# Performance work log

Hardware: AMD Instinct MI355X
Metric: run time of the kernel (lower is better)

## Reference

```python
import jax, jax.numpy as jnp
import numpy as np

# Model dims
B, T, E, H = 2, 2048, 512, 8
HEAD_DIM = E // H            # 64
NUM_SCALES = 4               # Gauss-Laguerre quadrature nodes
NUM_PRF = 16                 # positive random features per scale
POLY_DIM = 16                # degree-2 TensorSketch dim
EPS = 1e-5
CHUNK = 128                  # chunk size for exact chunked causal linear attention


def setup_inputs() -> dict:
    key = jax.random.key(0)
    ks = jax.random.split(key, 10)
    x = jax.random.normal(ks[0], (B, T, E), jnp.float32)
    sc = 1.0 / np.sqrt(E)  # xavier-ish scale for square projections
    Wq = jax.random.normal(ks[1], (E, E), jnp.float32) * sc
    Wk = jax.random.normal(ks[2], (E, E), jnp.float32) * sc
    Wv = jax.random.normal(ks[3], (E, E), jnp.float32) * sc
    Wo = jax.random.normal(ks[4], (E, E), jnp.float32) * sc
    # FAVOR+ gaussian projections, one block per quadrature scale
    projections = jax.random.normal(ks[5], (NUM_SCALES, NUM_PRF, HEAD_DIM), jnp.float32)
    # Gauss-Laguerre nodes/weights for 1/(C - 2 q.k) = int_0^inf exp(-t(C - 2 q.k)) dt
    nodes, weights = np.polynomial.laguerre.laggauss(NUM_SCALES)
    coef = weights * np.exp(nodes) * np.exp(-nodes * EPS)
    scales = jnp.asarray(np.stack([nodes, coef], axis=1), jnp.float32)  # [S, 2] = (t_s, c_s)
    # degree-2 TensorSketch (count-sketch hashes + rademacher signs)
    sketch_h = jax.random.randint(ks[6], (2, HEAD_DIM), 0, POLY_DIM)
    sketch_s = (jax.random.randint(ks[7], (2, HEAD_DIM), 0, 2) * 2 - 1).astype(jnp.float32)
    return dict(x=x, Wq=Wq, Wk=Wk, Wv=Wv, Wo=Wo, projections=projections,
                scales=scales, sketch_h=sketch_h, sketch_s=sketch_s)


def _features(u, projections, scales, sketch_h, sketch_s):
    """Multi-scale FAVOR+ x TensorSketch feature map for the spherical YAT kernel.

    u: [B,T,H,d], unit-normalized along d. Returns [B,T,H, P*S*m].
    Phi(q).Phi(k) ~= (q.k)^2 / (||q-k||^2 + eps).
    """
    t = scales[:, 0]  # quadrature nodes t_s
    c = scales[:, 1]  # quadrature coeffs w_s e^{t_s} e^{-t_s eps}
    S, m, d = projections.shape
    z = jnp.einsum('smd,bthd->bthsm', projections, u)
    # exp(2 t q.k) via positive RFs; extra e^{-t||u||^2}=e^{-t} (unit sphere) folded in -> -2t
    ef = jnp.exp(jnp.sqrt(2.0 * t)[:, None] * z - 2.0 * t[:, None]) * jnp.sqrt(c / m)[:, None]  # [B,T,H,S,m]
    # degree-2 TensorSketch: countsketch via one-hot matmul, combine with FFT conv
    M1 = sketch_s[0][:, None] * jax.nn.one_hot(sketch_h[0], POLY_DIM, dtype=u.dtype)  # [d,P]
    M2 = sketch_s[1][:, None] * jax.nn.one_hot(sketch_h[1], POLY_DIM, dtype=u.dtype)
    ts = jnp.fft.irfft(jnp.fft.rfft(u @ M1) * jnp.fft.rfft(u @ M2), n=POLY_DIM)  # [B,T,H,P]
    Bs, Ts, Hs = u.shape[:3]
    ef = ef.reshape(Bs, Ts, Hs, S * m)
    return (ts[..., :, None] * ef[..., None, :]).reshape(Bs, Ts, Hs, POLY_DIM * S * m)


def reference(x, Wq, Wk, Wv, Wo, projections, scales, sketch_h, sketch_s):
    Bx, Tx, Ex = x.shape
    d = HEAD_DIM
    q = (x @ Wq).reshape(Bx, Tx, H, d)
    k = (x @ Wk).reshape(Bx, Tx, H, d)
    v = (x @ Wv).reshape(Bx, Tx, H, d)
    # spherical: project q,k to unit sphere
    qn = q / (jnp.linalg.norm(q, axis=-1, keepdims=True) + 1e-6)
    kn = k / (jnp.linalg.norm(k, axis=-1, keepdims=True) + 1e-6)
    fq = _features(qn, projections, scales, sketch_h, sketch_s)  # [B,T,H,F]
    fk = _features(kn, projections, scales, sketch_h, sketch_s)
    F = fq.shape[-1]
    # exact chunked causal linear attention: O(T) state, no [T,T] matrix
    N = Tx // CHUNK
    fq_ = fq.reshape(Bx, N, CHUNK, H, F)
    fk_ = fk.reshape(Bx, N, CHUNK, H, F)
    v_ = v.reshape(Bx, N, CHUNK, H, d)
    kv = jnp.einsum('bnchf,bnchd->bnhfd', fk_, v_)   # per-chunk sum of phi(k) v^T
    kz = fk_.sum(axis=2)                              # [B,N,H,F]
    kv_prev = jnp.concatenate([jnp.zeros_like(kv[:, :1]), jnp.cumsum(kv, axis=1)[:, :-1]], axis=1)
    kz_prev = jnp.concatenate([jnp.zeros_like(kz[:, :1]), jnp.cumsum(kz, axis=1)[:, :-1]], axis=1)
    num = jnp.einsum('bnchf,bnhfd->bnchd', fq_, kv_prev)
    den = jnp.einsum('bnchf,bnhf->bnch', fq_, kz_prev)
    # intra-chunk causal part
    sc = jnp.einsum('bnchf,bnkhf->bnhck', fq_, fk_)
    mask = jnp.tril(jnp.ones((CHUNK, CHUNK), bool))
    scm = jnp.where(mask, sc, 0.0)
    num = num + jnp.einsum('bnhck,bnkhd->bnchd', scm, v_)
    den = den + jnp.swapaxes(scm.sum(axis=-1), 2, 3)
    out = num / (den[..., None] + EPS)
    out = out.reshape(Bx, Tx, Ex) @ Wo
    return out
```

## Files before the change

### kernel.cpp

```cpp
#include <hip/hip_runtime.h>
#include <math.h>

#define B_ 2
#define T_ 2048
#define E_ 512
#define H_ 8
#define D_ 64
#define NCH 16
#define CH 128
#define EPS_ 1e-5f

__global__ __launch_bounds__(256) void gemm512(const float* __restrict__ A,
                                               const float* __restrict__ W,
                                               float* __restrict__ C) {
  __shared__ float As[16][68];
  __shared__ float Bs[16][68];
  const int tid = threadIdx.x;
  const int tx = tid & 15, ty = tid >> 4;
  const int row0 = blockIdx.x * 64, col0 = blockIdx.y * 64;
  const int lr = tid >> 2, lk = (tid & 3) * 4;
  const int bkr = tid >> 4, bcc = (tid & 15) * 4;
  float acc[4][4] = {};
  for (int k0 = 0; k0 < 512; k0 += 16) {
    float4 a4 = *(const float4*)(A + (size_t)(row0 + lr) * 512 + k0 + lk);
    As[lk + 0][lr] = a4.x; As[lk + 1][lr] = a4.y;
    As[lk + 2][lr] = a4.z; As[lk + 3][lr] = a4.w;
    *(float4*)&Bs[bkr][bcc] = *(const float4*)(W + (size_t)(k0 + bkr) * 512 + col0 + bcc);
    __syncthreads();
#pragma unroll
    for (int kk = 0; kk < 16; ++kk) {
      float4 av = *(const float4*)&As[kk][ty * 4];
      float4 bv = *(const float4*)&Bs[kk][tx * 4];
      float aa[4] = {av.x, av.y, av.z, av.w};
      float bb[4] = {bv.x, bv.y, bv.z, bv.w};
#pragma unroll
      for (int i = 0; i < 4; ++i)
#pragma unroll
        for (int j = 0; j < 4; ++j) acc[i][j] += aa[i] * bb[j];
    }
    __syncthreads();
  }
#pragma unroll
  for (int i = 0; i < 4; ++i) {
    float4 o = make_float4(acc[i][0], acc[i][1], acc[i][2], acc[i][3]);
    *(float4*)(C + (size_t)(row0 + ty * 4 + i) * 512 + col0 + tx * 4) = o;
  }
}

__global__ __launch_bounds__(256) void feat_kernel(
    const float* __restrict__ q, const float* __restrict__ k,
    const float* __restrict__ proj, const float* __restrict__ scales,
    const int* __restrict__ sh, const float* __restrict__ ss,
    float* __restrict__ Tq, float* __restrict__ Eq,
    float* __restrict__ Tk, float* __restrict__ Ek) {
  __shared__ float Us[128][68];
  __shared__ float PjT[64][68];
  __shared__ float MT[64][36];
  __shared__ float Ps[128][36];
  __shared__ float csq[64], cmb[64], ccf[64];
  const int tid = threadIdx.x;
  const int isK = blockIdx.y;
  const float* in = (isK ? k : q) + (size_t)blockIdx.x * 8192;
  float* To = isK ? Tk : Tq;
  float* Eo = isK ? Ek : Eq;

#pragma unroll
  for (int j = 0; j < 8; ++j) {
    const int f = tid + 256 * j;
    float4 a = *(const float4*)(in + 4 * f);
    *(float4*)&Us[f >> 4][(f & 15) * 4] = a;
  }
  for (int i = tid; i < 4096; i += 256) PjT[i & 63][i >> 6] = proj[i];
  for (int i = tid; i < 64 * 36; i += 256) (&MT[0][0])[i] = 0.f;
  __syncthreads();

  if (tid < 64) {
    MT[tid][sh[tid]] = ss[tid];
    MT[tid][16 + sh[64 + tid]] = ss[64 + tid];
  } else if (tid < 128) {
    const int c = tid - 64;
    const float t = scales[(c >> 4) * 2], cc = scales[(c >> 4) * 2 + 1];
    csq[c] = sqrtf(2.f * t); cmb[c] = -2.f * t; ccf[c] = sqrtf(cc / 16.f);
  }
  {
    const int r2 = tid >> 1, hf = tid & 1;
    float4 tv[8]; float s2 = 0.f;
#pragma unroll
    for (int j2 = 0; j2 < 8; ++j2) {
      tv[j2] = *(const float4*)&Us[r2][hf * 32 + 4 * j2];
      s2 += tv[j2].x * tv[j2].x + tv[j2].y * tv[j2].y + tv[j2].z * tv[j2].z + tv[j2].w * tv[j2].w;
    }
    s2 += __shfl_xor(s2, 1);
    const float inv = 1.f / (sqrtf(s2) + 1e-6f);
#pragma unroll
    for (int j2 = 0; j2 < 8; ++j2) {
      tv[j2].x *= inv; tv[j2].y *= inv; tv[j2].z *= inv; tv[j2].w *= inv;
      *(float4*)&Us[r2][hf * 32 + 4 * j2] = tv[j2];
    }
  }
  __syncthreads();

  const int tx = tid & 7, ty = tid >> 3;
  const int c0 = tx * 8, pc0 = tx * 4;
  float accz[4][8] = {};
  float accp[4][4] = {};
  for (int d0 = 0; d0 < 64; d0 += 4) {
    float Aar[4][4];
#pragma unroll
    for (int i = 0; i < 4; ++i) {
      float4 a4 = *(const float4*)&Us[ty + 32 * i][d0];
      Aar[i][0] = a4.x; Aar[i][1] = a4.y; Aar[i][2] = a4.z; Aar[i][3] = a4.w;
    }
#pragma unroll
    for (int dd = 0; dd < 4; ++dd) {
      float4 bl = *(const float4*)&PjT[d0 + dd][c0];
      float4 bh = *(const float4*)&PjT[d0 + dd][c0 + 4];
      float4 bm = *(const float4*)&MT[d0 + dd][pc0];
      float bb[8] = {bl.x, bl.y, bl.z, bl.w, bh.x, bh.y, bh.z, bh.w};
      float bp[4] = {bm.x, bm.y, bm.z, bm.w};
#pragma unroll
      for (int i = 0; i < 4; ++i) {
        const float a = Aar[i][dd];
#pragma unroll
        for (int j = 0; j < 8; ++j) accz[i][j] += a * bb[j];
#pragma unroll
        for (int j = 0; j < 4; ++j) accp[i][j] += a * bp[j];
      }
    }
  }

  float sq8[8], mb8[8], cf8[8];
#pragma unroll
  for (int j = 0; j < 8; ++j) { sq8[j] = csq[c0 + j]; mb8[j] = cmb[c0 + j]; cf8[j] = ccf[c0 + j]; }
  const int bx16 = blockIdx.x * 16;
#pragma unroll
  for (int i = 0; i < 4; ++i) {
    const int r = ty + 32 * i;
    const int bt = bx16 + (r >> 3);
    const size_t orow = (size_t)((bt >> 11) * 8 + (r & 7)) * 2048 + (bt & 2047);
    float e[8];
#pragma unroll
    for (int j = 0; j < 8; ++j) e[j] = expf(sq8[j] * accz[i][j] + mb8[j]) * cf8[j];
    *(float4*)(Eo + orow * 64 + c0) = make_float4(e[0], e[1], e[2], e[3]);
    *(float4*)(Eo + orow * 64 + c0 + 4) = make_float4(e[4], e[5], e[6], e[7]);
    *(float4*)&Ps[r][pc0] = make_float4(accp[i][0], accp[i][1], accp[i][2], accp[i][3]);
  }
  __syncthreads();

  const int rr = tid >> 1, hf2 = tid & 1;
  float p1v[16], p2v[16];
#pragma unroll
  for (int j4 = 0; j4 < 4; ++j4) {
    float4 a = *(const float4*)&Ps[rr][j4 * 4];
    p1v[j4 * 4 + 0] = a.x; p1v[j4 * 4 + 1] = a.y; p1v[j4 * 4 + 2] = a.z; p1v[j4 * 4 + 3] = a.w;
    float4 b2 = *(const float4*)&Ps[rr][16 + j4 * 4];
    p2v[j4 * 4 + 0] = b2.x; p2v[j4 * 4 + 1] = b2.y; p2v[j4 * 4 + 2] = b2.z; p2v[j4 * 4 + 3] = b2.w;
  }
  const int bt2 = bx16 + (rr >> 3);
  const size_t orow2 = (size_t)((bt2 >> 11) * 8 + (rr & 7)) * 2048 + (bt2 & 2047);
  float tout[8];
  if (hf2 == 0) {
#pragma unroll
    for (int r8 = 0; r8 < 8; ++r8) {
      float a = 0.f;
#pragma unroll
      for (int j = 0; j < 16; ++j) a += p1v[j] * p2v[(r8 - j) & 15];
      tout[r8] = a;
    }
  } else {
#pragma unroll
    for (int r8 = 0; r8 < 8; ++r8) {
      float a = 0.f;
#pragma unroll
      for (int j = 0; j < 16; ++j) a += p1v[j] * p2v[(8 + r8 - j) & 15];
      tout[r8] = a;
    }
  }
  *(float4*)(To + orow2 * 16 + hf2 * 8) = make_float4(tout[0], tout[1], tout[2], tout[3]);
  *(float4*)(To + orow2 * 16 + hf2 * 8 + 4) = make_float4(tout[4], tout[5], tout[6], tout[7]);
}

__global__ __launch_bounds__(256) void vrelayout(const float* __restrict__ v, float* __restrict__ vh) {
  const int f = blockIdx.x * 256 + threadIdx.x;
  float4 a = *(const float4*)(v + 4 * (size_t)f);
  const int d4 = f & 15, h = (f >> 4) & 7, bt = f >> 7;
  const size_t orow = (size_t)((bt >> 11) * 8 + h) * 2048 + (bt & 2047);
  *(float4*)(vh + orow * 64 + d4 * 4) = a;
}

__global__ __launch_bounds__(256) void kv_kernel(const float* __restrict__ Tk, const float* __restrict__ Ek,
                                                 const float* __restrict__ vh, float* __restrict__ KV) {
  const int bhn = blockIdx.x;
  const int slice = blockIdx.y;
  __shared__ float tks[128][20];
  __shared__ float eks[128][16];
  __shared__ float vs[128][64];
  const int tid = threadIdx.x;
  const size_t rowbase = (size_t)bhn * 128;
  for (int i = tid; i < 2048; i += 256) tks[i >> 4][i & 15] = Tk[rowbase * 16 + i];
  for (int i = tid; i < 2048; i += 256) { int r = i >> 4, e = i & 15; eks[r][e] = Ek[(rowbase + r) * 64 + slice * 16 + e]; }
  for (int i = tid; i < 2048; i += 256) {
    float4 v4 = *(const float4*)(vh + rowbase * 64 + 4 * i);
    *(float4*)&vs[(4 * i) >> 6][(4 * i) & 63] = v4;
  }
  __syncthreads();
  const int d = tid & 63, er = tid >> 6;
  float acc[4][16] = {};
  for (int c = 0; c < 128; ++c) {
    float4 t0 = *(const float4*)&tks[c][0];
    float4 t1 = *(const float4*)&tks[c][4];
    float4 t2 = *(const float4*)&tks[c][8];
    float4 t3 = *(const float4*)&tks[c][12];
    float tkc[16] = {t0.x, t0.y, t0.z, t0.w, t1.x, t1.y, t1.z, t1.w,
                     t2.x, t2.y, t2.z, t2.w, t3.x, t3.y, t3.z, t3.w};
    float4 e4 = *(const float4*)&eks[c][er * 4];
    const float w = vs[c][d];
    float ai[4] = {e4.x * w, e4.y * w, e4.z * w, e4.w * w};
#pragma unroll
    for (int i = 0; i < 4; ++i)
#pragma unroll
      for (int p = 0; p < 16; ++p) acc[i][p] += tkc[p] * ai[i];
  }
  float* out = KV + (size_t)bhn * 65536;
#pragma unroll
  for (int i = 0; i < 4; ++i)
#pragma unroll
    for (int p = 0; p < 16; ++p)
      out[(size_t)(p * 64 + slice * 16 + er * 4 + i) * 64 + d] = acc[i][p];
}

__global__ __launch_bounds__(256) void kz_kernel(const float* __restrict__ Tk, const float* __restrict__ Ek,
                                                 float* __restrict__ KZ) {
  const int bhn = blockIdx.x;
  __shared__ float tks[128][20];
  __shared__ float eks[128][64];
  const int tid = threadIdx.x;
  const size_t rowbase = (size_t)bhn * 128;
  for (int i = tid; i < 2048; i += 256) tks[i >> 4][i & 15] = Tk[rowbase * 16 + i];
  for (int i = tid; i < 2048; i += 256) {
    float4 v4 = *(const float4*)(Ek + rowbase * 64 + 4 * i);
    *(float4*)&eks[(4 * i) >> 6][(4 * i) & 63] = v4;
  }
  __syncthreads();
  const int e = tid & 63, p0 = (tid >> 6) * 4;
  float a[4] = {};
  for (int c = 0; c < 128; ++c) {
    float4 t4 = *(const float4*)&tks[c][p0];
    const float ek = eks[c][e];
    a[0] += t4.x * ek; a[1] += t4.y * ek; a[2] += t4.z * ek; a[3] += t4.w * ek;
  }
#pragma unroll
  for (int j = 0; j < 4; ++j) KZ[(size_t)bhn * 1024 + (p0 + j) * 64 + e] = a[j];
}

__global__ void cumsum_kernel(float* __restrict__ KV, float* __restrict__ KZ) {
  const size_t idx = (size_t)blockIdx.x * 256 + threadIdx.x;
  const size_t nkv = (size_t)B_ * H_ * 65536;
  if (idx < nkv) {
    const size_t bh = idx >> 16, j = idx & 65535;
    float* p = KV + bh * NCH * 65536 + j;
    float a = 0.f;
#pragma unroll
    for (int n = 0; n < NCH; ++n) { const float t = p[(size_t)n << 16]; p[(size_t)n << 16] = a; a += t; }
  } else {
    const size_t i2 = idx - nkv;
    if (i2 < (size_t)B_ * H_ * 1024) {
      const size_t bh = i2 >> 10, j = i2 & 1023;
      float* p = KZ + bh * NCH * 1024 + j;
      float a = 0.f;
#pragma unroll
      for (int n = 0; n < NCH; ++n) { const float t = p[n << 10]; p[n << 10] = a; a += t; }
    }
  }
}

__global__ __launch_bounds__(256) void intra_kernel(const float* __restrict__ Tq, const float* __restrict__ Eq,
                                                    const float* __restrict__ Tk, const float* __restrict__ Ek,
                                                    const float* __restrict__ vh,
                                                    float* __restrict__ numb, float* __restrict__ den) {
  const int bhn = blockIdx.x;
  const int rh = blockIdx.y;
  __shared__ float tks[128][20];
  __shared__ float eks[128][68];
  __shared__ float vs[128][68];
  const int tid = threadIdx.x;
  const int r = tid >> 2, dg = tid & 3, d0 = dg * 16;
  const int nk = (rh + 1) * 64;
  const size_t chunkbase = (size_t)bhn * 128;
  const size_t myrow = chunkbase + rh * 64 + r;

  for (int i = tid; i < nk * 16; i += 256) tks[i >> 4][i & 15] = Tk[chunkbase * 16 + i];
  for (int i = tid; i < nk * 16; i += 256) {
    float4 e4 = *(const float4*)(Ek + chunkbase * 64 + 4 * i);
    *(float4*)&eks[(4 * i) >> 6][(4 * i) & 63] = e4;
    float4 w4 = *(const float4*)(vh + chunkbase * 64 + 4 * i);
    *(float4*)&vs[(4 * i) >> 6][(4 * i) & 63] = w4;
  }
  float tq[16], eq[64];
#pragma unroll
  for (int pp = 0; pp < 4; ++pp) {
    float4 t4 = *(const float4*)(Tq + myrow * 16 + pp * 4);
    tq[pp * 4 + 0] = t4.x; tq[pp * 4 + 1] = t4.y; tq[pp * 4 + 2] = t4.z; tq[pp * 4 + 3] = t4.w;
  }
#pragma unroll
  for (int ee = 0; ee < 16; ++ee) {
    float4 e4 = *(const float4*)(Eq + myrow * 64 + ee * 4);
    eq[ee * 4 + 0] = e4.x; eq[ee * 4 + 1] = e4.y; eq[ee * 4 + 2] = e4.z; eq[ee * 4 + 3] = e4.w;
  }
  __syncthreads();

  float num[16] = {};
  float dn = 0.f;
  const int kmax = rh * 64 + r;
  for (int kk = 0; kk <= kmax; ++kk) {
    float dT = 0.f, dE = 0.f;
#pragma unroll
    for (int pp = 0; pp < 4; ++pp) {
      float4 t4 = *(const float4*)&tks[kk][pp * 4];
      dT += tq[pp * 4 + 0] * t4.x + tq[pp * 4 + 1] * t4.y + tq[pp * 4 + 2] * t4.z + tq[pp * 4 + 3] * t4.w;
    }
#pragma unroll
    for (int ee = 0; ee < 16; ++ee) {
      float4 e4 = *(const float4*)&eks[kk][ee * 4];
      dE += eq[ee * 4 + 0] * e4.x + eq[ee * 4 + 1] * e4.y + eq[ee * 4 + 2] * e4.z + eq[ee * 4 + 3] * e4.w;
    }
    const float s = dT * dE;
    dn += s;
#pragma unroll
    for (int jj = 0; jj < 4; ++jj) {
      float4 v4 = *(const float4*)&vs[kk][d0 + jj * 4];
      num[jj * 4 + 0] += s * v4.x; num[jj * 4 + 1] += s * v4.y;
      num[jj * 4 + 2] += s * v4.z; num[jj * 4 + 3] += s * v4.w;
    }
  }
#pragma unroll
  for (int jj = 0; jj < 4; ++jj) {
    float4 o = make_float4(num[jj * 4 + 0], num[jj * 4 + 1], num[jj * 4 + 2], num[jj * 4 + 3]);
    *(float4*)(numb + myrow * 64 + d0 + jj * 4) = o;
  }
  if (dg == 0) den[myrow] = dn;
}

__global__ __launch_bounds__(256) void inter_kernel(const float* __restrict__ Tq, const float* __restrict__ Eq,
                                                    const float* __restrict__ KV, const float* __restrict__ KZ,
                                                    const float* __restrict__ numb, const float* __restrict__ den,
                                                    float* __restrict__ att) {
  const int bhn = blockIdx.x;
  const int rh = blockIdx.y;
  const int n = bhn & 15, bh = bhn >> 4;
  const int b = bh >> 3, h = bh & 7;
  __shared__ float tqs[64][17];
  __shared__ float eqs[64][68];
  __shared__ float kvp[64][68];
  __shared__ float kzp[64];
  const int tid = threadIdx.x;
  const int tx = tid & 15, ty = tid >> 4;
  const size_t rowbase = (size_t)bhn * 128 + rh * 64;
  for (int i = tid; i < 1024; i += 256) tqs[i >> 4][i & 15] = Tq[rowbase * 16 + i];
  for (int i = tid; i < 1024; i += 256) {
    float4 v4 = *(const float4*)(Eq + rowbase * 64 + 4 * i);
    *(float4*)&eqs[i >> 4][(i & 15) * 4] = v4;
  }
  const float* kvb = KV + (size_t)bhn * 65536;
  const float* kzb = KZ + (size_t)bhn * 1024;
  float acc[4][4] = {};
  float accd[4] = {};
  for (int p = 0; p < 16; ++p) {
    __syncthreads();
#pragma unroll
    for (int j = 0; j < 4; ++j) {
      const int f = tid + 256 * j;
      float4 v4 = *(const float4*)(kvb + p * 4096 + 4 * f);
      *(float4*)&kvp[f >> 4][(f & 15) * 4] = v4;
    }
    if (tid < 64) kzp[tid] = kzb[p * 64 + tid];
    __syncthreads();
    float tqv[4];
#pragma unroll
    for (int ci = 0; ci < 4; ++ci) tqv[ci] = tqs[ty + 16 * ci][p];
    for (int e0 = 0; e0 < 64; e0 += 4) {
      float4 kz4 = *(const float4*)&kzp[e0];
      float4 kv0 = *(const float4*)&kvp[e0 + 0][tx * 4];
      float4 kv1 = *(const float4*)&kvp[e0 + 1][tx * 4];
      float4 kv2 = *(const float4*)&kvp[e0 + 2][tx * 4];
      float4 kv3 = *(const float4*)&kvp[e0 + 3][tx * 4];
#pragma unroll
      for (int ci = 0; ci < 4; ++ci) {
        float4 eq4 = *(const float4*)&eqs[ty + 16 * ci][e0];
        const float a0 = tqv[ci] * eq4.x, a1 = tqv[ci] * eq4.y;
        const float a2 = tqv[ci] * eq4.z, a3 = tqv[ci] * eq4.w;
        acc[ci][0] += a0 * kv0.x; acc[ci][1] += a0 * kv0.y; acc[ci][2] += a0 * kv0.z; acc[ci][3] += a0 * kv0.w;
        acc[ci][0] += a1 * kv1.x; acc[ci][1] += a1 * kv1.y; acc[ci][2] += a1 * kv1.z; acc[ci][3] += a1 * kv1.w;
        acc[ci][0] += a2 * kv2.x; acc[ci][1] += a2 * kv2.y; acc[ci][2] += a2 * kv2.z; acc[ci][3] += a2 * kv2.w;
        acc[ci][0] += a3 * kv3.x; acc[ci][1] += a3 * kv3.y; acc[ci][2] += a3 * kv3.z; acc[ci][3] += a3 * kv3.w;
        accd[ci] += a0 * kz4.x + a1 * kz4.y + a2 * kz4.z + a3 * kz4.w;
      }
    }
  }
#pragma unroll
  for (int ci = 0; ci < 4; ++ci) {
    const int rloc = ty + 16 * ci;
    const size_t row = rowbase + rloc;
    const int t = n * 128 + rh * 64 + rloc;
    const float invd = 1.f / (den[row] + accd[ci] + EPS_);
    float4 nm = *(const float4*)(numb + row * 64 + tx * 4);
    float4 o;
    o.x = (nm.x + acc[ci][0]) * invd;
    o.y = (nm.y + acc[ci][1]) * invd;
    o.z = (nm.z + acc[ci][2]) * invd;
    o.w = (nm.w + acc[ci][3]) * invd;
    *(float4*)(att + (size_t)(b * T_ + t) * 512 + h * 64 + tx * 4) = o;
  }
}

extern "C" void kernel_launch(void* const* d_in, const int* in_sizes, int n_in,
                              void* d_out, int out_size, void* d_ws, size_t ws_size,
                              hipStream_t stream) {
  const float* x   = (const float*)d_in[0];
  const float* Wq  = (const float*)d_in[1];
  const float* Wk  = (const float*)d_in[2];
  const float* Wv  = (const float*)d_in[3];
  const float* Wo  = (const float*)d_in[4];
  const float* prj = (const float*)d_in[5];
  const float* scl = (const float*)d_in[6];
  const int*   shh = (const int*)d_in[7];
  const float* sss = (const float*)d_in[8];

  float* ws  = (float*)d_ws;
  float* q   = ws;
  float* k   = q + 2097152;
  float* v   = k + 2097152;
  float* Tq  = v + 2097152;
  float* Eq  = Tq + 524288;
  float* Tk  = Eq + 2097152;
  float* Ek  = Tk + 524288;
  float* vh  = Ek + 2097152;
  float* KV  = vh + 2097152;
  float* KZ  = KV + 16777216;
  float* nmb = KZ + 262144;
  float* den = nmb + 2097152;
  float* att = den + 32768;

  dim3 gg(64, 8);
  hipLaunchKernelGGL(gemm512, gg, dim3(256), 0, stream, x, Wq, q);
  hipLaunchKernelGGL(gemm512, gg, dim3(256), 0, stream, x, Wk, k);
  hipLaunchKernelGGL(gemm512, gg, dim3(256), 0, stream, x, Wv, v);
  hipLaunchKernelGGL(feat_kernel, dim3(256, 2), dim3(256), 0, stream,
                     q, k, prj, scl, shh, sss, Tq, Eq, Tk, Ek);
  hipLaunchKernelGGL(vrelayout, dim3(2048), dim3(256), 0, stream, v, vh);
  hipLaunchKernelGGL(kv_kernel, dim3(256, 4), dim3(256), 0, stream, Tk, Ek, vh, KV);
  hipLaunchKernelGGL(kz_kernel, dim3(256), dim3(256), 0, stream, Tk, Ek, KZ);
  hipLaunchKernelGGL(cumsum_kernel, dim3(4160), dim3(256), 0, stream, KV, KZ);
  hipLaunchKernelGGL(intra_kernel, dim3(256, 2), dim3(256), 0, stream, Tq, Eq, Tk, Ek, vh, nmb, den);
  hipLaunchKernelGGL(inter_kernel, dim3(256, 2), dim3(256), 0, stream, Tq, Eq, KV, KZ, nmb, den, att);
  hipLaunchKernelGGL(gemm512, gg, dim3(256), 0, stream, att, Wo, (float*)d_out);
}
```

Baseline: 406.6 us.

## Enlarge GEMM tile to 128x64 with register-prefetched global loads

The 512x512 projection GEMM now computes a 128x64 output tile per block, with 8x4 accumulators per thread instead of 4x4. This doubles arithmetic per shared-memory load and halves the grid. Global loads for the next k-slice are prefetched into registers while the current slice is computed, to hide memory latency. In exchange, register use rises and the grid shrinks to 256 blocks, which could reduce occupancy on a large GPU.

New measurement: 408.1 us. Within noise of the previous version (+0.4%).

```diff
diff --git a/kernel.cpp b/kernel.cpp
--- a/kernel.cpp
+++ b/kernel.cpp
@@ -13,37 +13,47 @@
 __global__ __launch_bounds__(256) void gemm512(const float* __restrict__ A,
                                                const float* __restrict__ W,
                                                float* __restrict__ C) {
-  __shared__ float As[16][68];
+  __shared__ float As[16][132];
   __shared__ float Bs[16][68];
   const int tid = threadIdx.x;
+  const int row0 = blockIdx.x * 128, col0 = blockIdx.y * 64;
+  const int ar = tid >> 1, ak = (tid & 1) * 8;
+  const int bk = tid >> 4, bc = (tid & 15) * 4;
   const int tx = tid & 15, ty = tid >> 4;
-  const int row0 = blockIdx.x * 64, col0 = blockIdx.y * 64;
-  const int lr = tid >> 2, lk = (tid & 3) * 4;
-  const int bkr = tid >> 4, bcc = (tid & 15) * 4;
-  float acc[4][4] = {};
+  float4 pa0, pa1, pb;
+  pa0 = *(const float4*)(A + (size_t)(row0 + ar) * 512 + ak);
+  pa1 = *(const float4*)(A + (size_t)(row0 + ar) * 512 + ak + 4);
+  pb  = *(const float4*)(W + (size_t)bk * 512 + col0 + bc);
+  float acc[8][4] = {};
   for (int k0 = 0; k0 < 512; k0 += 16) {
-    float4 a4 = *(const float4*)(A + (size_t)(row0 + lr) * 512 + k0 + lk);
-    As[lk + 0][lr] = a4.x; As[lk + 1][lr] = a4.y;
-    As[lk + 2][lr] = a4.z; As[lk + 3][lr] = a4.w;
-    *(float4*)&Bs[bkr][bcc] = *(const float4*)(W + (size_t)(k0 + bkr) * 512 + col0 + bcc);
     __syncthreads();
+    As[ak + 0][ar] = pa0.x; As[ak + 1][ar] = pa0.y; As[ak + 2][ar] = pa0.z; As[ak + 3][ar] = pa0.w;
+    As[ak + 4][ar] = pa1.x; As[ak + 5][ar] = pa1.y; As[ak + 6][ar] = pa1.z; As[ak + 7][ar] = pa1.w;
+    *(float4*)&Bs[bk][bc] = pb;
+    if (k0 < 496) {
+      pa0 = *(const float4*)(A + (size_t)(row0 + ar) * 512 + k0 + 16 + ak);
+      pa1 = *(const float4*)(A + (size_t)(row0 + ar) * 512 + k0 + 16 + ak + 4);
+      pb  = *(const float4*)(W + (size_t)(k0 + 16 + bk) * 512 + col0 + bc);
+    }
+    __syncthreads();
 #pragma unroll
     for (int kk = 0; kk < 16; ++kk) {
-      float4 av = *(const float4*)&As[kk][ty * 4];
-      float4 bv = *(const float4*)&Bs[kk][tx * 4];
-      float aa[4] = {av.x, av.y, av.z, av.w};
-      float bb[4] = {bv.x, bv.y, bv.z, bv.w};
-#pragma unroll
-      for (int i = 0; i < 4; ++i)
+      float4 a0 = *(const float4*)&As[kk][ty * 4];
+      float4 a1 = *(const float4*)&As[kk][ty * 4 + 64];
+      float4 b  = *(const float4*)&Bs[kk][tx * 4];
+      float aa[8] = {a0.x, a0.y, a0.z, a0.w, a1.x, a1.y, a1.z, a1.w};
+      float bb[4] = {b.x, b.y, b.z, b.w};
+#pragma unroll
+      for (int i = 0; i < 8; ++i)
 #pragma unroll
         for (int j = 0; j < 4; ++j) acc[i][j] += aa[i] * bb[j];
     }
-    __syncthreads();
-  }
-#pragma unroll
-  for (int i = 0; i < 4; ++i) {
-    float4 o = make_float4(acc[i][0], acc[i][1], acc[i][2], acc[i][3]);
-    *(float4*)(C + (size_t)(row0 + ty * 4 + i) * 512 + col0 + tx * 4) = o;
+  }
+#pragma unroll
+  for (int i = 0; i < 8; ++i) {
+    const int r = row0 + (i < 4 ? ty * 4 + i : 64 + ty * 4 + (i - 4));
+    *(float4*)(C + (size_t)r * 512 + col0 + tx * 4) =
+        make_float4(acc[i][0], acc[i][1], acc[i][2], acc[i][3]);
   }
 }
 
@@ -441,7 +451,7 @@
   float* den = nmb + 2097152;
   float* att = den + 32768;
 
-  dim3 gg(64, 8);
+  dim3 gg(32, 8);
   hipLaunchKernelGGL(gemm512, gg, dim3(256), 0, stream, x, Wq, q);
   hipLaunchKernelGGL(gemm512, gg, dim3(256), 0, stream, x, Wk, k);
   hipLaunchKernelGGL(gemm512, gg, dim3(256), 0, stream, x, Wv, v);
```
